# Optimization experiments

Measured on AMD Instinct MI355X. Metric: run time of the kernel, lower is better.

## Reference

```python
import jax, jax.numpy as jnp
import numpy as np

HIDDEN = 512

def flip_sequences(x, lengths):
    # flax sst2-style flip: reverse each sequence's first `length` items, padding stays at end
    B, T = x.shape[0], x.shape[1]
    idxs = (jnp.arange(T - 1, -1, -1)[None, :] + lengths[:, None]) % T  # [B,T]
    return x[jnp.arange(B)[:, None], idxs]

def lstm_scan(x, Wi, Wh, b):
    # x: [B,T,D] -> outputs [B,T,H]; flax OptimizedLSTMCell math (gate order i,f,g,o)
    B = x.shape[0]
    H = Wh.shape[0]
    xW = jnp.einsum('btd,dg->tbg', x, Wi) + b  # precompute input projections, time-major [T,B,4H]
    def step(carry, xw):
        c, h = carry
        gates = xw + h @ Wh
        i, f, g, o = jnp.split(gates, 4, axis=-1)
        c = jax.nn.sigmoid(f) * c + jax.nn.sigmoid(i) * jnp.tanh(g)
        h = jax.nn.sigmoid(o) * jnp.tanh(c)
        return (c, h), h
    init = (jnp.zeros((B, H), x.dtype), jnp.zeros((B, H), x.dtype))
    _, hs = jax.lax.scan(step, init, xW)  # hs: [T,B,H]
    return jnp.swapaxes(hs, 0, 1)

def setup_inputs() -> dict:
    key = jax.random.key(0)
    ks = jax.random.split(key, 8)
    B, T, D, H = 16, 2048, 512, HIDDEN
    s_in = 1.0 / np.sqrt(D)
    s_h = 1.0 / np.sqrt(H)
    return {
        'inputs': jax.random.normal(ks[0], (B, T, D), jnp.float32),
        'lengths': jax.random.randint(ks[1], (B,), 1, T + 1, jnp.int32),
        'Wi_f': jax.random.normal(ks[2], (D, 4 * H), jnp.float32) * s_in,
        'Wh_f': jax.random.normal(ks[3], (H, 4 * H), jnp.float32) * s_h,
        'b_f': jnp.zeros((4 * H,), jnp.float32),
        'Wi_b': jax.random.normal(ks[4], (D, 4 * H), jnp.float32) * s_in,
        'Wh_b': jax.random.normal(ks[5], (H, 4 * H), jnp.float32) * s_h,
        'b_b': jnp.zeros((4 * H,), jnp.float32),
    }

def reference(inputs, lengths, Wi_f, Wh_f, b_f, Wi_b, Wh_b, b_b):
    fwd = lstm_scan(inputs, Wi_f, Wh_f, b_f)  # [B,T,H]
    rev_in = flip_sequences(inputs, lengths)
    bwd = lstm_scan(rev_in, Wi_b, Wh_b, b_b)
    bwd = flip_sequences(bwd, lengths)
    return jnp.concatenate([fwd, bwd], axis=-1)  # [B,T,2H]
```

## Files before the change

### kernel.cpp

```cpp
#include <hip/hip_runtime.h>
#include <cstdint>
#include <cstddef>

#define T_SEQ 2048
#define BATCH 16
#define DIM   512
#define HID   512
#define KTOT  1024
#define NCOL  2048
#define APAD  8
#define AROW  (KTOT + APAD)

typedef __attribute__((ext_vector_type(8))) short          s8v;
typedef __attribute__((ext_vector_type(4))) float          f4v;
typedef __attribute__((ext_vector_type(4))) unsigned short h4v;

#define HXIDX(d, s, b, j) (((((d) * 2 + (s)) * BATCH + (b)) * HID) + (j))

__device__ __forceinline__ unsigned short f2b(float f) {
  unsigned u = __builtin_bit_cast(unsigned, f);
  return (unsigned short)((u + 0x7fffu + ((u >> 16) & 1u)) >> 16);
}

__global__ __launch_bounds__(256, 1)
void lstm_persist(const float* __restrict__ x, const int* __restrict__ lengths,
                  const float* __restrict__ Wi_f, const float* __restrict__ Wh_f,
                  const float* __restrict__ b_f,
                  const float* __restrict__ Wi_b, const float* __restrict__ Wh_b,
                  const float* __restrict__ b_b,
                  unsigned int* __restrict__ hx,
                  float* __restrict__ out) {
  __shared__ unsigned short A[BATCH][AROW];
  __shared__ float glds[4][BATCH][16];

  const int w    = (int)blockIdx.x;
  const int dir  = w >> 5;
  const int g    = w & 31;
  const int j0   = g * 16;
  const int tid  = (int)threadIdx.x;
  const int lane = tid & 63;
  const int wv   = tid >> 6;
  const int b    = tid >> 4;
  const int sub  = tid & 15;
  const int len  = lengths[b];

  const float* bias = dir ? b_b : b_f;
  const float bi = bias[0 * HID + j0 + sub];
  const float bf = bias[1 * HID + j0 + sub];
  const float bg = bias[2 * HID + j0 + sub];
  const float bo = bias[3 * HID + j0 + sub];

  s8v wfrag[32];
  {
    const float* Wi = dir ? Wi_b : Wi_f;
    const float* Wh = dir ? Wh_b : Wh_f;
    const int col = wv * HID + j0 + (lane & 15);
    const int kb  = (lane >> 4) * 8;
#pragma unroll
    for (int kc = 0; kc < 16; ++kc) {
      const float* src = Wi + (size_t)(kc * 32 + kb) * NCOL + col;
      s8v f;
#pragma unroll
      for (int j = 0; j < 8; ++j) f[j] = (short)f2b(src[(size_t)j * NCOL]);
      wfrag[kc] = f;
    }
#pragma unroll
    for (int kc = 0; kc < 16; ++kc) {
      const float* src = Wh + (size_t)(kc * 32 + kb) * NCOL + col;
      s8v f;
#pragma unroll
      for (int j = 0; j < 8; ++j) f[j] = (short)f2b(src[(size_t)j * NCOL]);
      wfrag[16 + kc] = f;
    }
  }

  float c_state = 0.f;
  const int arow = lane & 15;
  const int koff = (lane >> 4) * 8;

  {
    const int tau0 = dir ? ((T_SEQ - 1 + len) & (T_SEQ - 1)) : 0;
    const float* xrow = x + ((size_t)b * T_SEQ + tau0) * DIM;
#pragma unroll
    for (int r = 0; r < 8; ++r) {
      const int k = sub * 4 + r * 64;
      f4v v = *(const f4v*)(xrow + k);
      h4v p; p[0] = f2b(v[0]); p[1] = f2b(v[1]); p[2] = f2b(v[2]); p[3] = f2b(v[3]);
      *(h4v*)&A[b][k] = p;
      h4v z = (h4v){0, 0, 0, 0};
      *(h4v*)&A[b][DIM + k] = z;
    }
  }
  __syncthreads();

  for (int t = 0; t < T_SEQ; ++t) {
    const int tau = dir ? ((T_SEQ - 1 - t + len) & (T_SEQ - 1)) : t;
    const bool notlast = (t + 1 < T_SEQ);
    const unsigned e = (unsigned)(t + 1);

    f4v xv[8];
    if (notlast) {
      const int taun = dir ? ((T_SEQ - 2 - t + len) & (T_SEQ - 1)) : (t + 1);
      const float* xrow = x + ((size_t)b * T_SEQ + taun) * DIM;
#pragma unroll
      for (int r = 0; r < 8; ++r) xv[r] = *(const f4v*)(xrow + sub * 4 + r * 64);
    }

    f4v acc0 = {0.f,0.f,0.f,0.f}, acc1 = {0.f,0.f,0.f,0.f};
    f4v acc2 = {0.f,0.f,0.f,0.f}, acc3 = {0.f,0.f,0.f,0.f};
    {
      const unsigned short* ap = &A[arow][koff];
#pragma unroll
      for (int kc = 0; kc < 32; kc += 4) {
        s8v a0 = *(const s8v*)(ap + (kc + 0) * 32);
        s8v a1 = *(const s8v*)(ap + (kc + 1) * 32);
        s8v a2 = *(const s8v*)(ap + (kc + 2) * 32);
        s8v a3 = *(const s8v*)(ap + (kc + 3) * 32);
        acc0 = __builtin_amdgcn_mfma_f32_16x16x32_bf16(a0, wfrag[kc + 0], acc0, 0, 0, 0);
        acc1 = __builtin_amdgcn_mfma_f32_16x16x32_bf16(a1, wfrag[kc + 1], acc1, 0, 0, 0);
        acc2 = __builtin_amdgcn_mfma_f32_16x16x32_bf16(a2, wfrag[kc + 2], acc2, 0, 0, 0);
        acc3 = __builtin_amdgcn_mfma_f32_16x16x32_bf16(a3, wfrag[kc + 3], acc3, 0, 0, 0);
      }
    }
#pragma unroll
    for (int r = 0; r < 4; ++r)
      glds[wv][(lane >> 4) * 4 + r][lane & 15] = (acc0[r] + acc1[r]) + (acc2[r] + acc3[r]);
    __syncthreads();

    {
      const float gi = glds[0][b][sub] + bi;
      const float gf = glds[1][b][sub] + bf;
      const float gg = glds[2][b][sub] + bg;
      const float go = glds[3][b][sub] + bo;
      const float si = 1.f / (1.f + __expf(-gi));
      const float sf = 1.f / (1.f + __expf(-gf));
      const float so = 1.f / (1.f + __expf(-go));
      const float tg = 1.f - 2.f / (1.f + __expf(2.f * gg));
      c_state = sf * c_state + si * tg;
      const float tc = 1.f - 2.f / (1.f + __expf(2.f * c_state));
      const float h = so * tc;
      if (notlast) {
        const unsigned tagged = ((unsigned)f2b(h) << 16) | e;
        __hip_atomic_store(&hx[HXIDX(dir, e & 1, b, j0 + sub)], tagged,
                           __ATOMIC_RELAXED, __HIP_MEMORY_SCOPE_AGENT);
      }
      out[((size_t)b * T_SEQ + tau) * (2 * HID) + (size_t)dir * HID + j0 + sub] = h;
    }

    if (notlast) {
#pragma unroll
      for (int r = 0; r < 8; ++r) {
        const int k = sub * 4 + r * 64;
        h4v p; p[0] = f2b(xv[r][0]); p[1] = f2b(xv[r][1]);
               p[2] = f2b(xv[r][2]); p[3] = f2b(xv[r][3]);
        *(h4v*)&A[b][k] = p;
      }

      const unsigned* hrow = hx + HXIDX(dir, e & 1, b, 0);
      const unsigned long long msk = 0x0000FFFF0000FFFFULL;
      const unsigned long long pat = ((unsigned long long)e << 32) | e;
      unsigned long long hu[16];
      while (true) {
        bool ok = true;
#pragma unroll
        for (int r = 0; r < 8; ++r) {
          const int k = sub * 4 + r * 64;
          hu[2 * r]     = __hip_atomic_load((const unsigned long long*)(hrow + k),
                                            __ATOMIC_RELAXED, __HIP_MEMORY_SCOPE_AGENT);
          hu[2 * r + 1] = __hip_atomic_load((const unsigned long long*)(hrow + k) + 1,
                                            __ATOMIC_RELAXED, __HIP_MEMORY_SCOPE_AGENT);
          ok &= ((hu[2 * r] & msk) == pat) & ((hu[2 * r + 1] & msk) == pat);
        }
        if (ok) break;
        __builtin_amdgcn_s_sleep(1);
      }
#pragma unroll
      for (int r = 0; r < 8; ++r) {
        const int k = sub * 4 + r * 64;
        h4v p;
        p[0] = (unsigned short)(hu[2 * r] >> 16);
        p[1] = (unsigned short)(hu[2 * r] >> 48);
        p[2] = (unsigned short)(hu[2 * r + 1] >> 16);
        p[3] = (unsigned short)(hu[2 * r + 1] >> 48);
        *(h4v*)&A[b][DIM + k] = p;
      }
      __syncthreads();
    }
  }
}

extern "C" void kernel_launch(void* const* d_in, const int* in_sizes, int n_in,
                              void* d_out, int out_size, void* d_ws, size_t ws_size,
                              hipStream_t stream) {
  const float* x    = (const float*)d_in[0];
  const int*   len  = (const int*)d_in[1];
  const float* Wi_f = (const float*)d_in[2];
  const float* Wh_f = (const float*)d_in[3];
  const float* b_f  = (const float*)d_in[4];
  const float* Wi_b = (const float*)d_in[5];
  const float* Wh_b = (const float*)d_in[6];
  const float* b_b  = (const float*)d_in[7];
  float* out = (float*)d_out;
  unsigned int* hx = (unsigned int*)d_ws;

  hipMemsetAsync(d_ws, 0, (size_t)2 * 2 * BATCH * HID * 4, stream);
  hipLaunchKernelGGL(lstm_persist, dim3(64), dim3(256), 0, stream,
                     x, len, Wi_f, Wh_f, b_f, Wi_b, Wh_b, b_b, hx, out);
}
```

Before: 5.722 ms.

## Overlap next-step input projection with recurrence wait and remove gate LDS exchange

Splits the per-step GEMM into an input part and a recurrent part. The input projection for the next step is computed with MFMA while waiting for other blocks' hidden state, using a double-buffered x tile in LDS. It also remaps the weight columns so each wave holds all four gates for its units, which lets the gate exchange use lane shuffles instead of an LDS round trip and a barrier. This shortens the serial critical path per timestep, at the cost of more complex indexing and an extra x prefetch distance.

Measured after the change: 6.608 ms. 15.5% more time.

```diff
diff --git a/kernel.cpp b/kernel.cpp
--- a/kernel.cpp
+++ b/kernel.cpp
@@ -6,16 +6,14 @@
 #define BATCH 16
 #define DIM   512
 #define HID   512
-#define KTOT  1024
 #define NCOL  2048
-#define APAD  8
-#define AROW  (KTOT + APAD)
+#define XROW  520
 
 typedef __attribute__((ext_vector_type(8))) short          s8v;
 typedef __attribute__((ext_vector_type(4))) float          f4v;
 typedef __attribute__((ext_vector_type(4))) unsigned short h4v;
 
-#define HXIDX(d, s, b, j) (((((d) * 2 + (s)) * BATCH + (b)) * HID) + (j))
+#define HXBASE(d, s) (((size_t)((d) * 2 + (s)) * BATCH) * HID)
 
 __device__ __forceinline__ unsigned short f2b(float f) {
   unsigned u = __builtin_bit_cast(unsigned, f);
@@ -30,108 +28,130 @@
                   const float* __restrict__ b_b,
                   unsigned int* __restrict__ hx,
                   float* __restrict__ out) {
-  __shared__ unsigned short A[BATCH][AROW];
-  __shared__ float glds[4][BATCH][16];
+  __shared__ unsigned short Ax[2][BATCH][XROW];
+  __shared__ unsigned short Ah[BATCH][XROW];
 
   const int w    = (int)blockIdx.x;
   const int dir  = w >> 5;
-  const int g    = w & 31;
-  const int j0   = g * 16;
+  const int j0   = (w & 31) * 16;
   const int tid  = (int)threadIdx.x;
   const int lane = tid & 63;
   const int wv   = tid >> 6;
+
   const int b    = tid >> 4;
   const int sub  = tid & 15;
   const int len  = lengths[b];
 
+  const int bm   = 4 * (lane >> 4) + ((lane >> 2) & 3);
+  const int jm   = j0 + 4 * wv + (lane & 3);
+  const int lenm = lengths[bm];
+
   const float* bias = dir ? b_b : b_f;
-  const float bi = bias[0 * HID + j0 + sub];
-  const float bf = bias[1 * HID + j0 + sub];
-  const float bg = bias[2 * HID + j0 + sub];
-  const float bo = bias[3 * HID + j0 + sub];
-
-  s8v wfrag[32];
+  const float bi = bias[0 * HID + jm];
+  const float bf = bias[1 * HID + jm];
+  const float bg = bias[2 * HID + jm];
+  const float bo = bias[3 * HID + jm];
+
+  s8v wfi[16], wfh[16];
   {
     const float* Wi = dir ? Wi_b : Wi_f;
     const float* Wh = dir ? Wh_b : Wh_f;
-    const int col = wv * HID + j0 + (lane & 15);
-    const int kb  = (lane >> 4) * 8;
+    const int colW = ((lane >> 2) & 3) * HID + j0 + 4 * wv + (lane & 3);
+    const int kb   = (lane >> 4) * 8;
 #pragma unroll
     for (int kc = 0; kc < 16; ++kc) {
-      const float* src = Wi + (size_t)(kc * 32 + kb) * NCOL + col;
+      const float* src = Wi + (size_t)(kc * 32 + kb) * NCOL + colW;
       s8v f;
 #pragma unroll
       for (int j = 0; j < 8; ++j) f[j] = (short)f2b(src[(size_t)j * NCOL]);
-      wfrag[kc] = f;
+      wfi[kc] = f;
     }
 #pragma unroll
     for (int kc = 0; kc < 16; ++kc) {
-      const float* src = Wh + (size_t)(kc * 32 + kb) * NCOL + col;
+      const float* src = Wh + (size_t)(kc * 32 + kb) * NCOL + colW;
       s8v f;
 #pragma unroll
       for (int j = 0; j < 8; ++j) f[j] = (short)f2b(src[(size_t)j * NCOL]);
-      wfrag[16 + kc] = f;
-    }
-  }
-
-  float c_state = 0.f;
+      wfh[kc] = f;
+    }
+  }
+
   const int arow = lane & 15;
   const int koff = (lane >> 4) * 8;
 
-  {
-    const int tau0 = dir ? ((T_SEQ - 1 + len) & (T_SEQ - 1)) : 0;
-    const float* xrow = x + ((size_t)b * T_SEQ + tau0) * DIM;
+  auto taus = [&](int s) { return dir ? ((T_SEQ - 1 - s + len) & (T_SEQ - 1)) : s; };
+
+#pragma unroll
+  for (int bb = 0; bb < 2; ++bb) {
+    const float* xrow = x + ((size_t)b * T_SEQ + taus(bb)) * DIM;
 #pragma unroll
     for (int r = 0; r < 8; ++r) {
       const int k = sub * 4 + r * 64;
       f4v v = *(const f4v*)(xrow + k);
       h4v p; p[0] = f2b(v[0]); p[1] = f2b(v[1]); p[2] = f2b(v[2]); p[3] = f2b(v[3]);
-      *(h4v*)&A[b][k] = p;
-      h4v z = (h4v){0, 0, 0, 0};
-      *(h4v*)&A[b][DIM + k] = z;
+      *(h4v*)&Ax[bb][b][k] = p;
     }
   }
   __syncthreads();
 
+  f4v accx;
+  {
+    f4v d0 = {0,0,0,0}, d1 = {0,0,0,0}, d2 = {0,0,0,0}, d3 = {0,0,0,0};
+    const unsigned short* ap = &Ax[0][arow][koff];
+#pragma unroll
+    for (int kc = 0; kc < 16; kc += 4) {
+      d0 = __builtin_amdgcn_mfma_f32_16x16x32_bf16(*(const s8v*)(ap + (kc+0)*32), wfi[kc+0], d0, 0,0,0);
+      d1 = __builtin_amdgcn_mfma_f32_16x16x32_bf16(*(const s8v*)(ap + (kc+1)*32), wfi[kc+1], d1, 0,0,0);
+      d2 = __builtin_amdgcn_mfma_f32_16x16x32_bf16(*(const s8v*)(ap + (kc+2)*32), wfi[kc+2], d2, 0,0,0);
+      d3 = __builtin_amdgcn_mfma_f32_16x16x32_bf16(*(const s8v*)(ap + (kc+3)*32), wfi[kc+3], d3, 0,0,0);
+    }
+    accx = (d0 + d1) + (d2 + d3);
+  }
+
+  float c_state = 0.f;
+
   for (int t = 0; t < T_SEQ; ++t) {
-    const int tau = dir ? ((T_SEQ - 1 - t + len) & (T_SEQ - 1)) : t;
+    const unsigned e = (unsigned)(t + 1);
     const bool notlast = (t + 1 < T_SEQ);
-    const unsigned e = (unsigned)(t + 1);
 
     f4v xv[8];
     if (notlast) {
-      const int taun = dir ? ((T_SEQ - 2 - t + len) & (T_SEQ - 1)) : (t + 1);
-      const float* xrow = x + ((size_t)b * T_SEQ + taun) * DIM;
+      const int tsn = (t + 2 < T_SEQ) ? (t + 2) : 0;
+      const float* xrow = x + ((size_t)b * T_SEQ + taus(tsn)) * DIM;
 #pragma unroll
       for (int r = 0; r < 8; ++r) xv[r] = *(const f4v*)(xrow + sub * 4 + r * 64);
     }
 
-    f4v acc0 = {0.f,0.f,0.f,0.f}, acc1 = {0.f,0.f,0.f,0.f};
-    f4v acc2 = {0.f,0.f,0.f,0.f}, acc3 = {0.f,0.f,0.f,0.f};
-    {
-      const unsigned short* ap = &A[arow][koff];
-#pragma unroll
-      for (int kc = 0; kc < 32; kc += 4) {
-        s8v a0 = *(const s8v*)(ap + (kc + 0) * 32);
-        s8v a1 = *(const s8v*)(ap + (kc + 1) * 32);
-        s8v a2 = *(const s8v*)(ap + (kc + 2) * 32);
-        s8v a3 = *(const s8v*)(ap + (kc + 3) * 32);
-        acc0 = __builtin_amdgcn_mfma_f32_16x16x32_bf16(a0, wfrag[kc + 0], acc0, 0, 0, 0);
-        acc1 = __builtin_amdgcn_mfma_f32_16x16x32_bf16(a1, wfrag[kc + 1], acc1, 0, 0, 0);
-        acc2 = __builtin_amdgcn_mfma_f32_16x16x32_bf16(a2, wfrag[kc + 2], acc2, 0, 0, 0);
-        acc3 = __builtin_amdgcn_mfma_f32_16x16x32_bf16(a3, wfrag[kc + 3], acc3, 0, 0, 0);
-      }
-    }
-#pragma unroll
-    for (int r = 0; r < 4; ++r)
-      glds[wv][(lane >> 4) * 4 + r][lane & 15] = (acc0[r] + acc1[r]) + (acc2[r] + acc3[r]);
-    __syncthreads();
-
-    {
-      const float gi = glds[0][b][sub] + bi;
-      const float gf = glds[1][b][sub] + bf;
-      const float gg = glds[2][b][sub] + bg;
-      const float go = glds[3][b][sub] + bo;
+    f4v acc = accx;
+    if (t > 0) {
+      f4v c1 = {0,0,0,0}, c2 = {0,0,0,0}, c3 = {0,0,0,0};
+      const unsigned short* ap = &Ah[arow][koff];
+#pragma unroll
+      for (int kc = 0; kc < 16; kc += 4) {
+        acc = __builtin_amdgcn_mfma_f32_16x16x32_bf16(*(const s8v*)(ap + (kc+0)*32), wfh[kc+0], acc, 0,0,0);
+        c1  = __builtin_amdgcn_mfma_f32_16x16x32_bf16(*(const s8v*)(ap + (kc+1)*32), wfh[kc+1], c1,  0,0,0);
+        c2  = __builtin_amdgcn_mfma_f32_16x16x32_bf16(*(const s8v*)(ap + (kc+2)*32), wfh[kc+2], c2,  0,0,0);
+        c3  = __builtin_amdgcn_mfma_f32_16x16x32_bf16(*(const s8v*)(ap + (kc+3)*32), wfh[kc+3], c3,  0,0,0);
+      }
+      acc = (acc + c1) + (c2 + c3);
+    }
+
+    {
+      const int gb0 = (lane >> 2) & 1;
+      float t0 = __shfl_xor(gb0 ? acc[0] : acc[1], 4);
+      float t1 = __shfl_xor(gb0 ? acc[2] : acc[3], 4);
+      if (gb0) { acc[0] = t0; acc[2] = t1; } else { acc[1] = t0; acc[3] = t1; }
+      const int gb1 = (lane >> 3) & 1;
+      float u0 = __shfl_xor(gb1 ? acc[0] : acc[2], 8);
+      float u1 = __shfl_xor(gb1 ? acc[1] : acc[3], 8);
+      if (gb1) { acc[0] = u0; acc[1] = u1; } else { acc[2] = u0; acc[3] = u1; }
+    }
+
+    {
+      const float gi = acc[0] + bi;
+      const float gf = acc[1] + bf;
+      const float gg = acc[2] + bg;
+      const float go = acc[3] + bo;
       const float si = 1.f / (1.f + __expf(-gi));
       const float sf = 1.f / (1.f + __expf(-gf));
       const float so = 1.f / (1.f + __expf(-go));
@@ -141,51 +161,80 @@
       const float h = so * tc;
       if (notlast) {
         const unsigned tagged = ((unsigned)f2b(h) << 16) | e;
-        __hip_atomic_store(&hx[HXIDX(dir, e & 1, b, j0 + sub)], tagged,
+        __hip_atomic_store(&hx[HXBASE(dir, e & 1) + (size_t)bm * HID + jm], tagged,
                            __ATOMIC_RELAXED, __HIP_MEMORY_SCOPE_AGENT);
       }
-      out[((size_t)b * T_SEQ + tau) * (2 * HID) + (size_t)dir * HID + j0 + sub] = h;
-    }
-
-    if (notlast) {
-#pragma unroll
-      for (int r = 0; r < 8; ++r) {
-        const int k = sub * 4 + r * 64;
-        h4v p; p[0] = f2b(xv[r][0]); p[1] = f2b(xv[r][1]);
-               p[2] = f2b(xv[r][2]); p[3] = f2b(xv[r][3]);
-        *(h4v*)&A[b][k] = p;
-      }
-
-      const unsigned* hrow = hx + HXIDX(dir, e & 1, b, 0);
+      const int tauo = dir ? ((T_SEQ - 1 - t + lenm) & (T_SEQ - 1)) : t;
+      out[((size_t)bm * T_SEQ + tauo) * (2 * HID) + (size_t)dir * HID + jm] = h;
+    }
+
+    if (!notlast) break;
+
+    __syncthreads();
+
+    const unsigned* hrow = hx + HXBASE(dir, e & 1) + (size_t)b * HID;
+    unsigned long long hu[16];
+#pragma unroll
+    for (int r = 0; r < 8; ++r) {
+      const int k = sub * 4 + r * 64;
+      hu[2*r]   = __hip_atomic_load((const unsigned long long*)(hrow + k),
+                                    __ATOMIC_RELAXED, __HIP_MEMORY_SCOPE_AGENT);
+      hu[2*r+1] = __hip_atomic_load((const unsigned long long*)(hrow + k) + 1,
+                                    __ATOMIC_RELAXED, __HIP_MEMORY_SCOPE_AGENT);
+    }
+
+    {
+      f4v d0 = {0,0,0,0}, d1 = {0,0,0,0}, d2 = {0,0,0,0}, d3 = {0,0,0,0};
+      const unsigned short* ap = &Ax[(t + 1) & 1][arow][koff];
+#pragma unroll
+      for (int kc = 0; kc < 16; kc += 4) {
+        d0 = __builtin_amdgcn_mfma_f32_16x16x32_bf16(*(const s8v*)(ap + (kc+0)*32), wfi[kc+0], d0, 0,0,0);
+        d1 = __builtin_amdgcn_mfma_f32_16x16x32_bf16(*(const s8v*)(ap + (kc+1)*32), wfi[kc+1], d1, 0,0,0);
+        d2 = __builtin_amdgcn_mfma_f32_16x16x32_bf16(*(const s8v*)(ap + (kc+2)*32), wfi[kc+2], d2, 0,0,0);
+        d3 = __builtin_amdgcn_mfma_f32_16x16x32_bf16(*(const s8v*)(ap + (kc+3)*32), wfi[kc+3], d3, 0,0,0);
+      }
+      accx = (d0 + d1) + (d2 + d3);
+    }
+
+#pragma unroll
+    for (int r = 0; r < 8; ++r) {
+      const int k = sub * 4 + r * 64;
+      h4v p; p[0] = f2b(xv[r][0]); p[1] = f2b(xv[r][1]);
+             p[2] = f2b(xv[r][2]); p[3] = f2b(xv[r][3]);
+      *(h4v*)&Ax[t & 1][b][k] = p;
+    }
+
+    {
       const unsigned long long msk = 0x0000FFFF0000FFFFULL;
       const unsigned long long pat = ((unsigned long long)e << 32) | e;
-      unsigned long long hu[16];
       while (true) {
         bool ok = true;
 #pragma unroll
+        for (int r = 0; r < 16; ++r) ok &= ((hu[r] & msk) == pat);
+        if (ok) break;
+        __builtin_amdgcn_s_sleep(1);
+#pragma unroll
         for (int r = 0; r < 8; ++r) {
           const int k = sub * 4 + r * 64;
-          hu[2 * r]     = __hip_atomic_load((const unsigned long long*)(hrow + k),
-                                            __ATOMIC_RELAXED, __HIP_MEMORY_SCOPE_AGENT);
-          hu[2 * r + 1] = __hip_atomic_load((const unsigned long long*)(hrow + k) + 1,
-                                            __ATOMIC_RELAXED, __HIP_MEMORY_SCOPE_AGENT);
-          ok &= ((hu[2 * r] & msk) == pat) & ((hu[2 * r + 1] & msk) == pat);
+          hu[2*r]   = __hip_atomic_load((const unsigned long long*)(hrow + k),
+                                        __ATOMIC_RELAXED, __HIP_MEMORY_SCOPE_AGENT);
+          hu[2*r+1] = __hip_atomic_load((const unsigned long long*)(hrow + k) + 1,
+                                        __ATOMIC_RELAXED, __HIP_MEMORY_SCOPE_AGENT);
         }
-        if (ok) break;
-        __builtin_amdgcn_s_sleep(1);
-      }
-#pragma unroll
-      for (int r = 0; r < 8; ++r) {
-        const int k = sub * 4 + r * 64;
-        h4v p;
-        p[0] = (unsigned short)(hu[2 * r] >> 16);
-        p[1] = (unsigned short)(hu[2 * r] >> 48);
-        p[2] = (unsigned short)(hu[2 * r + 1] >> 16);
-        p[3] = (unsigned short)(hu[2 * r + 1] >> 48);
-        *(h4v*)&A[b][DIM + k] = p;
-      }
-      __syncthreads();
-    }
+      }
+    }
+
+#pragma unroll
+    for (int r = 0; r < 8; ++r) {
+      const int k = sub * 4 + r * 64;
+      h4v p;
+      p[0] = (unsigned short)(hu[2*r]   >> 16);
+      p[1] = (unsigned short)(hu[2*r]   >> 48);
+      p[2] = (unsigned short)(hu[2*r+1] >> 16);
+      p[3] = (unsigned short)(hu[2*r+1] >> 48);
+      *(h4v*)&Ah[b][k] = p;
+    }
+    __syncthreads();
   }
 }
 
```
